# Optimization experiments

Hardware: AMD Instinct MI355X
Metric: run time of the kernel (lower is better)

The kernel has to match this reference:

```python
import jax, jax.numpy as jnp
import numpy as np

B, I, O, G = 4096, 256, 256, 8
GRID_MIN, GRID_MAX, RHO = -2.0, 2.0, 1.0


def setup_inputs() -> dict:
    key = jax.random.key(0)
    ks = jax.random.split(key, 8)
    return {
        "x_re": jax.random.normal(ks[0], (B, I), dtype=jnp.float32),
        "x_im": jax.random.normal(ks[1], (B, I), dtype=jnp.float32),
        "realweights": jax.random.normal(ks[2], (I, O, G, G), dtype=jnp.float32),
        "complexweights": jax.random.normal(ks[3], (I, O, G, G), dtype=jnp.float32),
        "silu_weight_re": jax.random.normal(ks[4], (I, O), dtype=jnp.float32),
        "silu_weight_im": jax.random.normal(ks[5], (I, O), dtype=jnp.float32),
        "silu_bias_re": 0.1 * jax.random.normal(ks[6], (I, O), dtype=jnp.float32),
        "silu_bias_im": 0.1 * jax.random.normal(ks[7], (I, O), dtype=jnp.float32),
    }


def reference(x_re, x_im, realweights, complexweights,
              silu_weight_re, silu_weight_im, silu_bias_re, silu_bias_im):
    # Complex grid: grid[u, v] = lin[u] + i * lin[v]
    lin = jnp.linspace(GRID_MIN, GRID_MAX, G, dtype=x_re.dtype)
    # |x - grid|^2 = (x_re - lin_u)^2 + (x_im - lin_v)^2  -> (B, I, G, G)
    dre = x_re[:, :, None, None] - lin[None, None, :, None]
    dim = x_im[:, :, None, None] - lin[None, None, None, :]
    basis = jnp.exp(-(dre * dre + dim * dim) / RHO)  # real-valued (B, I, G, G)
    # RBF contraction: real and imaginary output channels
    out_re = jnp.einsum('biuv,iouv->bo', basis, realweights)
    out_im = jnp.einsum('biuv,iouv->bo', basis, complexweights)
    # Complex SiLU (complex_weight variant): silu applied component-wise,
    # then complex-multiplied by silu_weight, plus bias, summed over i.
    s_re = jax.nn.silu(x_re)  # (B, I)
    s_im = jax.nn.silu(x_im)
    out_re = out_re + s_re @ silu_weight_re - s_im @ silu_weight_im + jnp.sum(silu_bias_re, axis=0)
    out_im = out_im + s_im @ silu_weight_re + s_re @ silu_weight_im + jnp.sum(silu_bias_im, axis=0)
    # Return complex output as stacked (real, imag): (B, O, 2)
    return jnp.stack([out_re, out_im], axis=-1)
```

## Files before the change

### kernel.cpp

```cpp
#include <hip/hip_runtime.h>
#include <hip/hip_fp16.h>
#include <stdint.h>

typedef float floatx4 __attribute__((ext_vector_type(4)));
typedef short short8 __attribute__((ext_vector_type(8)));

constexpr int I_SZ = 256, O_SZ = 256, NCOL = 512, B_SZ = 4096;
constexpr int KSTEPS = 264;
constexpr float GSTEP = 4.0f / 7.0f;
constexpr float NLOG2E = -1.44269504088896f;

__device__ __forceinline__ uint32_t pk_bf16(float lo, float hi) {
  return __builtin_amdgcn_perm(__float_as_uint(hi), __float_as_uint(lo), 0x07060302u);
}
__device__ __forceinline__ short rne_bf16(float f) {
  uint32_t u = __float_as_uint(f);
  return (short)((u + 0x7FFFu + ((u >> 16) & 1u)) >> 16);
}

__device__ __forceinline__ void gload_lds16(const void* g, void* l) {
  __builtin_amdgcn_global_load_lds((const __attribute__((address_space(1))) void*)g,
                                   (__attribute__((address_space(3))) void*)l,
                                   16, 0, 0);
}

__device__ __forceinline__ float silu_f(float a) {
  return a * __builtin_amdgcn_rcpf(1.f + __builtin_amdgcn_exp2f(a * NLOG2E));
}

__global__ void pack_weights(const float* __restrict__ rw, const float* __restrict__ cw,
                             const float* __restrict__ swre, const float* __restrict__ swim,
                             short* __restrict__ wpack) {
  int idx = blockIdx.x * 256 + threadIdx.x;
  int kb = idx >> 12;
  int rem = idx & 4095;
  int n = rem >> 3, gp = rem & 7;
  int g = gp ^ (n & 7);
  int o = n >> 1, c = n & 1;
  float w[8];
  if (kb < 256) {
    const float* W = (c ? cw : rw) + (((size_t)kb * O_SZ + o) << 6) + (g << 3);
    float4 a = *(const float4*)W;
    float4 b = *(const float4*)(W + 4);
    w[0] = a.x; w[1] = a.y; w[2] = a.z; w[3] = a.w;
    w[4] = b.x; w[5] = b.y; w[6] = b.z; w[7] = b.w;
  } else {
    int kp0 = ((kb - 256) << 6) + (g << 3);
    #pragma unroll
    for (int e = 0; e < 8; ++e) {
      int kp = kp0 + e, i = kp >> 1, ci = kp & 1;
      float a = swre[i * O_SZ + o], b = swim[i * O_SZ + o];
      w[e] = (c == 0) ? (ci == 0 ? a : -b) : (ci == 0 ? b : a);
    }
  }
  uint32_t h[8];
  #pragma unroll
  for (int e = 0; e < 8; ++e) h[e] = (uint32_t)(uint16_t)rne_bf16(w[e]);
  uint4 val = make_uint4(h[0] | (h[1] << 16), h[2] | (h[3] << 16),
                         h[4] | (h[5] << 16), h[6] | (h[7] << 16));
  *(uint4*)(wpack + (size_t)idx * 8) = val;
}

__global__ void transpose_x(const float* __restrict__ xre, const float* __restrict__ xim,
                            __half* __restrict__ xT) {
  __shared__ float tile[64][65];
  int bt = blockIdx.x & 63;
  int it = (blockIdx.x >> 6) & 3;
  int c  = blockIdx.x >> 8;
  const float* src = (c ? xim : xre);
  int b0 = bt << 6, i0 = it << 6;
  int t = threadIdx.x;
  int il = t & 63, bh = t >> 6;
  #pragma unroll
  for (int k = 0; k < 16; ++k) {
    int bl = bh + (k << 2);
    tile[bl][il] = src[(size_t)(b0 + bl) * I_SZ + i0 + il];
  }
  __syncthreads();
  int bl2 = t & 63, ih = t >> 6;
  __half* dst = xT + ((size_t)c * I_SZ + i0) * B_SZ + b0;
  #pragma unroll
  for (int k = 0; k < 16; ++k) {
    int il2 = ih + (k << 2);
    dst[(size_t)il2 * B_SZ + bl2] = __float2half(tile[bl2][il2]);
  }
}

__global__ void bias_sums(const float* __restrict__ bre, const float* __restrict__ bim,
                          float* __restrict__ bsum) {
  int n = blockIdx.x, o = n >> 1, l = threadIdx.x;
  const float* src = ((n & 1) ? bim : bre) + o;
  float s = 0.f;
  #pragma unroll
  for (int a = 0; a < 4; ++a) s += src[(size_t)(a * 64 + l) * O_SZ];
  #pragma unroll
  for (int off = 32; off; off >>= 1) s += __shfl_down(s, off, 64);
  if (l == 0) bsum[n] = s;
}

__global__ __launch_bounds__(256, 4) void cvkan_gemm(
    const float* __restrict__ xre, const float* __restrict__ xim,
    const __half* __restrict__ xT,
    const short* __restrict__ wpack, const float* __restrict__ bsum,
    float* __restrict__ out) {
  __shared__ __align__(16) short Bs[128 * 64];
  __shared__ __align__(16) short As[128 * 64];

  const int tid = threadIdx.x;
  const int bid = blockIdx.x;
  const int kch = bid & 7;
  const int mn = bid >> 3;
  const int mt = mn >> 2, nt = mn & 3;
  const int b0 = mt * 128, n0 = nt * 128;
  const int l = tid & 63, w = tid >> 6;
  const int wr = w >> 1, wc = w & 1;
  const int lm = l & 15, q = l >> 4;
  const int r = tid >> 1, h = tid & 1;

  const __half* xTre = xT;
  const __half* xTim = xT + (size_t)I_SZ * B_SZ;

  floatx4 acc[4][4] = {};

  for (int j = 0; j < 33; ++j) {
    const int s = (j < 32) ? (kch * 32 + j) : (256 + kch);

    float xr = 0.f, xi = 0.f;
    if (j < 32) {
      xr = __half2float(xTre[(size_t)s * B_SZ + b0 + r]);
      xi = __half2float(xTim[(size_t)s * B_SZ + b0 + r]);
    }

    {
      const short* src = wpack + (((size_t)s * NCOL + n0) << 6) + (tid << 3);
      short* ldst = Bs + (w << 9);
      gload_lds16(src,        ldst);
      gload_lds16(src + 2048, ldst + 2048);
      gload_lds16(src + 4096, ldst + 4096);
      gload_lds16(src + 6144, ldst + 6144);
    }

    if (j < 32) {
      float eiv[8];
      #pragma unroll
      for (int v = 0; v < 8; ++v) {
        float d = xi - (-2.0f + v * GSTEP);
        eiv[v] = __builtin_amdgcn_exp2f(d * d * NLOG2E);
      }
      #pragma unroll
      for (int uu = 0; uu < 4; ++uu) {
        int u = h * 4 + uu;
        float d = xr - (-2.0f + u * GSTEP);
        float er = __builtin_amdgcn_exp2f(d * d * NLOG2E);
        uint4 val = make_uint4(pk_bf16(er * eiv[0], er * eiv[1]),
                               pk_bf16(er * eiv[2], er * eiv[3]),
                               pk_bf16(er * eiv[4], er * eiv[5]),
                               pk_bf16(er * eiv[6], er * eiv[7]));
        *(uint4*)(As + (r << 6) + ((u ^ (r & 7)) << 3)) = val;
      }
    } else {
      int sl = kch;
      #pragma unroll
      for (int gg = 0; gg < 4; ++gg) {
        int g = h * 4 + gg;
        const float* pr = xre + (size_t)(b0 + r) * I_SZ + (sl << 5) + (g << 2);
        const float* pi = xim + (size_t)(b0 + r) * I_SZ + (sl << 5) + (g << 2);
        uint4 val = make_uint4(pk_bf16(silu_f(pr[0]), silu_f(pi[0])),
                               pk_bf16(silu_f(pr[1]), silu_f(pi[1])),
                               pk_bf16(silu_f(pr[2]), silu_f(pi[2])),
                               pk_bf16(silu_f(pr[3]), silu_f(pi[3])));
        *(uint4*)(As + (r << 6) + ((g ^ (r & 7)) << 3)) = val;
      }
    }

    __builtin_amdgcn_s_waitcnt(0);
    __syncthreads();

    short8 bf[4][2];
    #pragma unroll
    for (int nn = 0; nn < 4; ++nn) {
      int col = wc * 64 + nn * 16 + lm;
      const short* bp = Bs + (col << 6);
      bf[nn][0] = *(const short8*)(bp + ((q       ^ (col & 7)) << 3));
      bf[nn][1] = *(const short8*)(bp + (((q + 4) ^ (col & 7)) << 3));
    }
    #pragma unroll
    for (int mm = 0; mm < 4; ++mm) {
      int row = wr * 64 + mm * 16 + lm;
      const short* ap = As + (row << 6);
      short8 a0 = *(const short8*)(ap + ((q       ^ (row & 7)) << 3));
      short8 a1 = *(const short8*)(ap + (((q + 4) ^ (row & 7)) << 3));
      #pragma unroll
      for (int nn = 0; nn < 4; ++nn) {
        acc[mm][nn] = __builtin_amdgcn_mfma_f32_16x16x32_bf16(a0, bf[nn][0], acc[mm][nn], 0, 0, 0);
        acc[mm][nn] = __builtin_amdgcn_mfma_f32_16x16x32_bf16(a1, bf[nn][1], acc[mm][nn], 0, 0, 0);
      }
    }
    __syncthreads();
  }

  #pragma unroll
  for (int nn = 0; nn < 4; ++nn) {
    int col = n0 + wc * 64 + nn * 16 + lm;
    float bv = (kch == 7) ? bsum[col] : 0.0f;
    #pragma unroll
    for (int mm = 0; mm < 4; ++mm) {
      int row0 = b0 + wr * 64 + mm * 16 + (q << 2);
      #pragma unroll
      for (int r2 = 0; r2 < 4; ++r2)
        atomicAdd(out + (size_t)(row0 + r2) * NCOL + col, acc[mm][nn][r2] + bv);
    }
  }
}

extern "C" void kernel_launch(void* const* d_in, const int* in_sizes, int n_in,
                              void* d_out, int out_size, void* d_ws, size_t ws_size,
                              hipStream_t stream) {
  const float* xre  = (const float*)d_in[0];
  const float* xim  = (const float*)d_in[1];
  const float* rw   = (const float*)d_in[2];
  const float* cw   = (const float*)d_in[3];
  const float* swre = (const float*)d_in[4];
  const float* swim = (const float*)d_in[5];
  const float* bre  = (const float*)d_in[6];
  const float* bim  = (const float*)d_in[7];
  float* out = (float*)d_out;

  size_t wpack_bytes = (size_t)KSTEPS * NCOL * 64 * 2;
  short* wpack = (short*)d_ws;
  float* bsum  = (float*)((char*)d_ws + wpack_bytes);
  __half* xT   = (__half*)((char*)d_ws + wpack_bytes + 2048);

  hipMemsetAsync(d_out, 0, (size_t)B_SZ * NCOL * sizeof(float), stream);
  pack_weights<<<(KSTEPS * NCOL * 8) / 256, 256, 0, stream>>>(rw, cw, swre, swim, wpack);
  transpose_x<<<512, 256, 0, stream>>>(xre, xim, xT);
  bias_sums<<<NCOL, 64, 0, stream>>>(bre, bim, bsum);
  cvkan_gemm<<<1024, 256, 0, stream>>>(xre, xim, xT, wpack, bsum, out);
}
```

Baseline: 207.5 us.

## Enlarge GEMM tiles to 128x256 and software-pipeline A/B staging

The main kernel now uses 512-thread blocks with a 128x256 output tile and a 4-way K split instead of 8, so the grid drops from 1024 blocks to 256. B tiles are triple-buffered through direct global-to-LDS loads, and A (RBF basis) tiles are double-buffered and built one step ahead. Each step ends with a partial vmcnt wait and a single barrier instead of a full drain and two syncs, and MFMA priority is raised during compute. The aim is to overlap weight loads and basis generation with matrix math and to halve the atomic output traffic. In exchange, more LDS is used per block and only 256 blocks run, which may underfill the GPU.

```diff
diff --git a/kernel.cpp b/kernel.cpp
--- a/kernel.cpp
+++ b/kernel.cpp
@@ -98,49 +98,48 @@
   if (l == 0) bsum[n] = s;
 }
 
-__global__ __launch_bounds__(256, 4) void cvkan_gemm(
+__global__ __launch_bounds__(512, 2) void cvkan_gemm(
     const float* __restrict__ xre, const float* __restrict__ xim,
     const __half* __restrict__ xT,
     const short* __restrict__ wpack, const float* __restrict__ bsum,
     float* __restrict__ out) {
-  __shared__ __align__(16) short Bs[128 * 64];
-  __shared__ __align__(16) short As[128 * 64];
+  __shared__ __align__(16) short As[2 * 128 * 64];
+  __shared__ __align__(16) short Bs[3 * 256 * 64];
 
   const int tid = threadIdx.x;
   const int bid = blockIdx.x;
-  const int kch = bid & 7;
-  const int mn = bid >> 3;
-  const int mt = mn >> 2, nt = mn & 3;
-  const int b0 = mt * 128, n0 = nt * 128;
+  const int kch = bid & 3;
+  const int mn = bid >> 2;
+  const int mt = mn >> 1, nt = mn & 1;
+  const int b0 = mt * 128, n0 = nt * 256;
   const int l = tid & 63, w = tid >> 6;
-  const int wr = w >> 1, wc = w & 1;
+  const int wr = w >> 2, wc = w & 3;
   const int lm = l & 15, q = l >> 4;
-  const int r = tid >> 1, h = tid & 1;
+  const int r = tid >> 2, p = tid & 3;
 
   const __half* xTre = xT;
   const __half* xTim = xT + (size_t)I_SZ * B_SZ;
 
+  short* ac = As;       short* an  = As + 8192;
+  short* bc = Bs;       short* bn1 = Bs + 16384;   short* bn2 = Bs + 32768;
+
   floatx4 acc[4][4] = {};
 
-  for (int j = 0; j < 33; ++j) {
-    const int s = (j < 32) ? (kch * 32 + j) : (256 + kch);
-
-    float xr = 0.f, xi = 0.f;
-    if (j < 32) {
-      xr = __half2float(xTre[(size_t)s * B_SZ + b0 + r]);
-      xi = __half2float(xTim[(size_t)s * B_SZ + b0 + r]);
-    }
-
-    {
-      const short* src = wpack + (((size_t)s * NCOL + n0) << 6) + (tid << 3);
-      short* ldst = Bs + (w << 9);
-      gload_lds16(src,        ldst);
-      gload_lds16(src + 2048, ldst + 2048);
-      gload_lds16(src + 4096, ldst + 4096);
-      gload_lds16(src + 6144, ldst + 6144);
-    }
-
-    if (j < 32) {
+  auto sidx = [&](int j) { return j < 64 ? kch * 64 + j : 256 + kch * 2 + (j - 64); };
+
+  auto stage_B = [&](short* bdst, int s) {
+    const short* src = wpack + (((size_t)s * NCOL + n0) << 6) + (tid << 3);
+    short* ldst = bdst + (w << 9);
+    gload_lds16(src,         ldst);
+    gload_lds16(src +  4096, ldst +  4096);
+    gload_lds16(src +  8192, ldst +  8192);
+    gload_lds16(src + 12288, ldst + 12288);
+  };
+
+  auto build_A = [&](short* adst, int s) {
+    if (s < 256) {
+      float xr = __half2float(xTre[(size_t)s * B_SZ + b0 + r]);
+      float xi = __half2float(xTim[(size_t)s * B_SZ + b0 + r]);
       float eiv[8];
       #pragma unroll
       for (int v = 0; v < 8; ++v) {
@@ -148,46 +147,55 @@
         eiv[v] = __builtin_amdgcn_exp2f(d * d * NLOG2E);
       }
       #pragma unroll
-      for (int uu = 0; uu < 4; ++uu) {
-        int u = h * 4 + uu;
+      for (int uu = 0; uu < 2; ++uu) {
+        int u = p * 2 + uu;
         float d = xr - (-2.0f + u * GSTEP);
         float er = __builtin_amdgcn_exp2f(d * d * NLOG2E);
         uint4 val = make_uint4(pk_bf16(er * eiv[0], er * eiv[1]),
                                pk_bf16(er * eiv[2], er * eiv[3]),
                                pk_bf16(er * eiv[4], er * eiv[5]),
                                pk_bf16(er * eiv[6], er * eiv[7]));
-        *(uint4*)(As + (r << 6) + ((u ^ (r & 7)) << 3)) = val;
+        *(uint4*)(adst + (r << 6) + ((u ^ (r & 7)) << 3)) = val;
       }
     } else {
-      int sl = kch;
-      #pragma unroll
-      for (int gg = 0; gg < 4; ++gg) {
-        int g = h * 4 + gg;
+      int sl = s - 256;
+      #pragma unroll
+      for (int gg = 0; gg < 2; ++gg) {
+        int g = p * 2 + gg;
         const float* pr = xre + (size_t)(b0 + r) * I_SZ + (sl << 5) + (g << 2);
         const float* pi = xim + (size_t)(b0 + r) * I_SZ + (sl << 5) + (g << 2);
         uint4 val = make_uint4(pk_bf16(silu_f(pr[0]), silu_f(pi[0])),
                                pk_bf16(silu_f(pr[1]), silu_f(pi[1])),
                                pk_bf16(silu_f(pr[2]), silu_f(pi[2])),
                                pk_bf16(silu_f(pr[3]), silu_f(pi[3])));
-        *(uint4*)(As + (r << 6) + ((g ^ (r & 7)) << 3)) = val;
-      }
-    }
-
-    __builtin_amdgcn_s_waitcnt(0);
-    __syncthreads();
+        *(uint4*)(adst + (r << 6) + ((g ^ (r & 7)) << 3)) = val;
+      }
+    }
+  };
+
+  stage_B(bc, sidx(0));
+  stage_B(bn1, sidx(1));
+  build_A(ac, sidx(0));
+  asm volatile("s_waitcnt vmcnt(4) lgkmcnt(0)" ::: "memory");
+  __builtin_amdgcn_s_barrier();
+
+  for (int j = 0; j < 66; ++j) {
+    if (j < 64) stage_B(bn2, sidx(j + 2));
+    if (j < 65) build_A(an, sidx(j + 1));
 
     short8 bf[4][2];
     #pragma unroll
     for (int nn = 0; nn < 4; ++nn) {
       int col = wc * 64 + nn * 16 + lm;
-      const short* bp = Bs + (col << 6);
+      const short* bp = bc + (col << 6);
       bf[nn][0] = *(const short8*)(bp + ((q       ^ (col & 7)) << 3));
       bf[nn][1] = *(const short8*)(bp + (((q + 4) ^ (col & 7)) << 3));
     }
+    __builtin_amdgcn_s_setprio(1);
     #pragma unroll
     for (int mm = 0; mm < 4; ++mm) {
       int row = wr * 64 + mm * 16 + lm;
-      const short* ap = As + (row << 6);
+      const short* ap = ac + (row << 6);
       short8 a0 = *(const short8*)(ap + ((q       ^ (row & 7)) << 3));
       short8 a1 = *(const short8*)(ap + (((q + 4) ^ (row & 7)) << 3));
       #pragma unroll
@@ -196,13 +204,21 @@
         acc[mm][nn] = __builtin_amdgcn_mfma_f32_16x16x32_bf16(a1, bf[nn][1], acc[mm][nn], 0, 0, 0);
       }
     }
-    __syncthreads();
+    __builtin_amdgcn_s_setprio(0);
+
+    if (j < 65) {
+      if (j < 64) asm volatile("s_waitcnt vmcnt(4) lgkmcnt(0)" ::: "memory");
+      else        asm volatile("s_waitcnt vmcnt(0) lgkmcnt(0)" ::: "memory");
+      __builtin_amdgcn_s_barrier();
+    }
+    short* t = bc; bc = bn1; bn1 = bn2; bn2 = t;
+    t = ac; ac = an; an = t;
   }
 
   #pragma unroll
   for (int nn = 0; nn < 4; ++nn) {
     int col = n0 + wc * 64 + nn * 16 + lm;
-    float bv = (kch == 7) ? bsum[col] : 0.0f;
+    float bv = (kch == 3) ? bsum[col] : 0.0f;
     #pragma unroll
     for (int mm = 0; mm < 4; ++mm) {
       int row0 = b0 + wr * 64 + mm * 16 + (q << 2);
@@ -235,5 +251,5 @@
   pack_weights<<<(KSTEPS * NCOL * 8) / 256, 256, 0, stream>>>(rw, cw, swre, swim, wpack);
   transpose_x<<<512, 256, 0, stream>>>(xre, xim, xT);
   bias_sums<<<NCOL, 64, 0, stream>>>(bre, bim, bsum);
-  cvkan_gemm<<<1024, 256, 0, stream>>>(xre, xim, xT, wpack, bsum, out);
-}
+  cvkan_gemm<<<256, 512, 0, stream>>>(xre, xim, xT, wpack, bsum, out);
+}
```

Result: slower. 223.0 us (+7.5%).

## Double-buffer B tiles and compute next A tile in registers during MFMA

Applied to the files above, without the earlier changes.

Double-buffers the weight tile in LDS so the async global-to-LDS load for the next K-step is issued before the current step's MFMAs. The next step's RBF basis is computed into registers while the MFMAs run, and x values are prefetched one step ahead. The global load is then waited on with a partial vmcnt instead of a full drain, and s_setprio raises wave priority around the MFMA block. The larger LDS footprint lowers the launch bound from 4 to 3 blocks per CU, so occupancy may drop and the hand-written waitcnt counts must stay exactly right.

```diff
diff --git a/kernel.cpp b/kernel.cpp
--- a/kernel.cpp
+++ b/kernel.cpp
@@ -98,13 +98,13 @@
   if (l == 0) bsum[n] = s;
 }
 
-__global__ __launch_bounds__(256, 4) void cvkan_gemm(
+__global__ __launch_bounds__(256, 3) void cvkan_gemm(
     const float* __restrict__ xre, const float* __restrict__ xim,
     const __half* __restrict__ xT,
     const short* __restrict__ wpack, const float* __restrict__ bsum,
     float* __restrict__ out) {
-  __shared__ __align__(16) short Bs[128 * 64];
   __shared__ __align__(16) short As[128 * 64];
+  __shared__ __align__(16) short Bs[2 * 128 * 64];
 
   const int tid = threadIdx.x;
   const int bid = blockIdx.x;
@@ -121,26 +121,21 @@
   const __half* xTim = xT + (size_t)I_SZ * B_SZ;
 
   floatx4 acc[4][4] = {};
-
-  for (int j = 0; j < 33; ++j) {
-    const int s = (j < 32) ? (kch * 32 + j) : (256 + kch);
-
-    float xr = 0.f, xi = 0.f;
-    if (j < 32) {
-      xr = __half2float(xTre[(size_t)s * B_SZ + b0 + r]);
-      xi = __half2float(xTim[(size_t)s * B_SZ + b0 + r]);
-    }
-
-    {
-      const short* src = wpack + (((size_t)s * NCOL + n0) << 6) + (tid << 3);
-      short* ldst = Bs + (w << 9);
-      gload_lds16(src,        ldst);
-      gload_lds16(src + 2048, ldst + 2048);
-      gload_lds16(src + 4096, ldst + 4096);
-      gload_lds16(src + 6144, ldst + 6144);
-    }
-
-    if (j < 32) {
+  uint4 rA[4];
+
+  auto sidx = [&](int j) { return (j < 32) ? (kch * 32 + j) : (256 + kch); };
+
+  auto stage_B = [&](short* bdst, int s) {
+    const short* src = wpack + (((size_t)s * NCOL + n0) << 6) + (tid << 3);
+    short* ldst = bdst + (w << 9);
+    gload_lds16(src,        ldst);
+    gload_lds16(src + 2048, ldst + 2048);
+    gload_lds16(src + 4096, ldst + 4096);
+    gload_lds16(src + 6144, ldst + 6144);
+  };
+
+  auto build_A = [&](int s, float xr, float xi) {
+    if (s < 256) {
       float eiv[8];
       #pragma unroll
       for (int v = 0; v < 8; ++v) {
@@ -152,38 +147,73 @@
         int u = h * 4 + uu;
         float d = xr - (-2.0f + u * GSTEP);
         float er = __builtin_amdgcn_exp2f(d * d * NLOG2E);
-        uint4 val = make_uint4(pk_bf16(er * eiv[0], er * eiv[1]),
-                               pk_bf16(er * eiv[2], er * eiv[3]),
-                               pk_bf16(er * eiv[4], er * eiv[5]),
-                               pk_bf16(er * eiv[6], er * eiv[7]));
-        *(uint4*)(As + (r << 6) + ((u ^ (r & 7)) << 3)) = val;
+        rA[uu] = make_uint4(pk_bf16(er * eiv[0], er * eiv[1]),
+                            pk_bf16(er * eiv[2], er * eiv[3]),
+                            pk_bf16(er * eiv[4], er * eiv[5]),
+                            pk_bf16(er * eiv[6], er * eiv[7]));
       }
     } else {
-      int sl = kch;
+      int sl = s - 256;
       #pragma unroll
       for (int gg = 0; gg < 4; ++gg) {
         int g = h * 4 + gg;
         const float* pr = xre + (size_t)(b0 + r) * I_SZ + (sl << 5) + (g << 2);
         const float* pi = xim + (size_t)(b0 + r) * I_SZ + (sl << 5) + (g << 2);
-        uint4 val = make_uint4(pk_bf16(silu_f(pr[0]), silu_f(pi[0])),
-                               pk_bf16(silu_f(pr[1]), silu_f(pi[1])),
-                               pk_bf16(silu_f(pr[2]), silu_f(pi[2])),
-                               pk_bf16(silu_f(pr[3]), silu_f(pi[3])));
-        *(uint4*)(As + (r << 6) + ((g ^ (r & 7)) << 3)) = val;
-      }
-    }
-
-    __builtin_amdgcn_s_waitcnt(0);
-    __syncthreads();
+        rA[gg] = make_uint4(pk_bf16(silu_f(pr[0]), silu_f(pi[0])),
+                            pk_bf16(silu_f(pr[1]), silu_f(pi[1])),
+                            pk_bf16(silu_f(pr[2]), silu_f(pi[2])),
+                            pk_bf16(silu_f(pr[3]), silu_f(pi[3])));
+      }
+    }
+  };
+
+  auto write_A = [&]() {
+    #pragma unroll
+    for (int uu = 0; uu < 4; ++uu) {
+      int u = h * 4 + uu;
+      *(uint4*)(As + (r << 6) + ((u ^ (r & 7)) << 3)) = rA[uu];
+    }
+  };
+
+  stage_B(Bs, sidx(0));
+  {
+    int s0 = sidx(0);
+    float xr = __half2float(xTre[(size_t)s0 * B_SZ + b0 + r]);
+    float xi = __half2float(xTim[(size_t)s0 * B_SZ + b0 + r]);
+    build_A(s0, xr, xi);
+  }
+
+  short* bcur = Bs;
+  short* bnxt = Bs + 8192;
+
+  for (int j = 0; j <= 32; ++j) {
+    const int sn = sidx(j + 1);
+
+    float xrn = 0.f, xin = 0.f;
+    if (j < 32 && sn < 256) {
+      xrn = __half2float(xTre[(size_t)sn * B_SZ + b0 + r]);
+      xin = __half2float(xTim[(size_t)sn * B_SZ + b0 + r]);
+    }
+    __builtin_amdgcn_sched_barrier(0);
+
+    if (j < 32) stage_B(bnxt, sn);
+    write_A();
+
+    if (j < 32) asm volatile("s_waitcnt vmcnt(4) lgkmcnt(0)" ::: "memory");
+    else        asm volatile("s_waitcnt vmcnt(0) lgkmcnt(0)" ::: "memory");
+    __builtin_amdgcn_s_barrier();
+
+    if (j < 32) build_A(sn, xrn, xin);
 
     short8 bf[4][2];
     #pragma unroll
     for (int nn = 0; nn < 4; ++nn) {
       int col = wc * 64 + nn * 16 + lm;
-      const short* bp = Bs + (col << 6);
+      const short* bp = bcur + (col << 6);
       bf[nn][0] = *(const short8*)(bp + ((q       ^ (col & 7)) << 3));
       bf[nn][1] = *(const short8*)(bp + (((q + 4) ^ (col & 7)) << 3));
     }
+    __builtin_amdgcn_s_setprio(1);
     #pragma unroll
     for (int mm = 0; mm < 4; ++mm) {
       int row = wr * 64 + mm * 16 + lm;
@@ -196,7 +226,10 @@
         acc[mm][nn] = __builtin_amdgcn_mfma_f32_16x16x32_bf16(a1, bf[nn][1], acc[mm][nn], 0, 0, 0);
       }
     }
-    __syncthreads();
+    __builtin_amdgcn_s_setprio(0);
+
+    if (j < 32) __builtin_amdgcn_s_barrier();
+    short* t = bcur; bcur = bnxt; bnxt = t;
   }
 
   #pragma unroll
```

Result: slower. 228.1 us (+9.9%).

## Double-buffer weight tiles, compute RBF A-fragments in registers, widen N tile

Applied to the files above, without the earlier changes.

The GEMM now uses a 128x256 output tile per block with two LDS buffers for the weight tile, prefetching the next K-step's weights and x values while the current step runs its MFMAs. The RBF basis is computed directly into A-operand registers per lane, so the A shared-memory tile and one barrier per step go away. MFMAs are wrapped in s_setprio. The aim is to overlap loads with compute and cut LDS traffic and syncs. In exchange there are more accumulators and registers, occupancy drops to 2 blocks, the grid is halved, and lanes sharing a row recompute exp values redundantly.

```diff
diff --git a/kernel.cpp b/kernel.cpp
--- a/kernel.cpp
+++ b/kernel.cpp
@@ -98,110 +98,138 @@
   if (l == 0) bsum[n] = s;
 }
 
-__global__ __launch_bounds__(256, 4) void cvkan_gemm(
+__global__ __launch_bounds__(256, 2) void cvkan_gemm(
     const float* __restrict__ xre, const float* __restrict__ xim,
     const __half* __restrict__ xT,
     const short* __restrict__ wpack, const float* __restrict__ bsum,
     float* __restrict__ out) {
-  __shared__ __align__(16) short Bs[128 * 64];
-  __shared__ __align__(16) short As[128 * 64];
+  __shared__ __align__(16) short Bs[2][256 * 64];
 
   const int tid = threadIdx.x;
   const int bid = blockIdx.x;
   const int kch = bid & 7;
   const int mn = bid >> 3;
-  const int mt = mn >> 2, nt = mn & 3;
-  const int b0 = mt * 128, n0 = nt * 128;
+  const int mt = mn >> 1, nt = mn & 1;
+  const int b0 = mt * 128, n0 = nt * 256;
   const int l = tid & 63, w = tid >> 6;
   const int wr = w >> 1, wc = w & 1;
   const int lm = l & 15, q = l >> 4;
-  const int r = tid >> 1, h = tid & 1;
+  const float gq  = -2.0f + q * GSTEP;
+  const float gq4 = gq + 4.0f * GSTEP;
 
   const __half* xTre = xT;
   const __half* xTim = xT + (size_t)I_SZ * B_SZ;
 
-  floatx4 acc[4][4] = {};
-
-  for (int j = 0; j < 33; ++j) {
-    const int s = (j < 32) ? (kch * 32 + j) : (256 + kch);
-
-    float xr = 0.f, xi = 0.f;
-    if (j < 32) {
-      xr = __half2float(xTre[(size_t)s * B_SZ + b0 + r]);
-      xi = __half2float(xTim[(size_t)s * B_SZ + b0 + r]);
-    }
-
-    {
-      const short* src = wpack + (((size_t)s * NCOL + n0) << 6) + (tid << 3);
-      short* ldst = Bs + (w << 9);
-      gload_lds16(src,        ldst);
-      gload_lds16(src + 2048, ldst + 2048);
-      gload_lds16(src + 4096, ldst + 4096);
-      gload_lds16(src + 6144, ldst + 6144);
-    }
-
-    if (j < 32) {
-      float eiv[8];
-      #pragma unroll
-      for (int v = 0; v < 8; ++v) {
-        float d = xi - (-2.0f + v * GSTEP);
-        eiv[v] = __builtin_amdgcn_exp2f(d * d * NLOG2E);
+  floatx4 acc[4][8] = {};
+
+  auto stage_B = [&](short* bdst, int s) {
+    const short* src = wpack + (((size_t)s * NCOL + n0) << 6) + (tid << 3);
+    short* ldst = bdst + (w << 9);
+    #pragma unroll
+    for (int rnd = 0; rnd < 8; ++rnd)
+      gload_lds16(src + rnd * 2048, ldst + rnd * 2048);
+  };
+
+  float xrc[4], xic[4];
+  auto load_x = [&](int s, float* xr, float* xi) {
+    #pragma unroll
+    for (int mm = 0; mm < 4; ++mm) {
+      int row = b0 + wr * 64 + mm * 16 + lm;
+      xr[mm] = __half2float(xTre[(size_t)s * B_SZ + row]);
+      xi[mm] = __half2float(xTim[(size_t)s * B_SZ + row]);
+    }
+  };
+
+  {
+    int s0 = kch * 32;
+    load_x(s0, xrc, xic);
+    stage_B(&Bs[0][0], s0);
+    asm volatile("s_waitcnt vmcnt(0) lgkmcnt(0)" ::: "memory");
+  }
+  __syncthreads();
+
+  for (int t = 0; t < 33; ++t) {
+    const bool last = (t == 32);
+    float xrn[4], xin[4];
+    if (t < 31) load_x(kch * 32 + t + 1, xrn, xin);
+    if (t < 32) stage_B(&Bs[(t + 1) & 1][0], (t + 1 < 32) ? (kch * 32 + t + 1) : (256 + kch));
+    __builtin_amdgcn_sched_barrier(0);
+
+    const short* bb = &Bs[t & 1][0];
+
+    short8 bf[8];
+    #pragma unroll
+    for (int nn = 0; nn < 8; ++nn) {
+      int colL = wc * 128 + nn * 16 + lm;
+      bf[nn] = *(const short8*)(bb + (colL << 6) + ((q ^ (colL & 7)) << 3));
+    }
+    short8 afh[4];
+    #pragma unroll
+    for (int mm = 0; mm < 4; ++mm) {
+      short8 alo;
+      if (!last) {
+        float eiv[8];
+        #pragma unroll
+        for (int v = 0; v < 8; ++v) {
+          float d = xic[mm] - (-2.0f + v * GSTEP);
+          eiv[v] = __builtin_amdgcn_exp2f(d * d * NLOG2E);
+        }
+        float d0 = xrc[mm] - gq;
+        float er = __builtin_amdgcn_exp2f(d0 * d0 * NLOG2E);
+        float d1 = xrc[mm] - gq4;
+        float e4 = __builtin_amdgcn_exp2f(d1 * d1 * NLOG2E);
+        uint4 va = make_uint4(pk_bf16(er * eiv[0], er * eiv[1]), pk_bf16(er * eiv[2], er * eiv[3]),
+                              pk_bf16(er * eiv[4], er * eiv[5]), pk_bf16(er * eiv[6], er * eiv[7]));
+        uint4 vh = make_uint4(pk_bf16(e4 * eiv[0], e4 * eiv[1]), pk_bf16(e4 * eiv[2], e4 * eiv[3]),
+                              pk_bf16(e4 * eiv[4], e4 * eiv[5]), pk_bf16(e4 * eiv[6], e4 * eiv[7]));
+        alo = *(short8*)&va; afh[mm] = *(short8*)&vh;
+      } else {
+        int row = b0 + wr * 64 + mm * 16 + lm;
+        const float* pr = xre + (size_t)row * I_SZ + (kch << 5);
+        const float* pi = xim + (size_t)row * I_SZ + (kch << 5);
+        uint4 va = make_uint4(pk_bf16(silu_f(pr[q * 4 + 0]), silu_f(pi[q * 4 + 0])),
+                              pk_bf16(silu_f(pr[q * 4 + 1]), silu_f(pi[q * 4 + 1])),
+                              pk_bf16(silu_f(pr[q * 4 + 2]), silu_f(pi[q * 4 + 2])),
+                              pk_bf16(silu_f(pr[q * 4 + 3]), silu_f(pi[q * 4 + 3])));
+        uint4 vh = make_uint4(pk_bf16(silu_f(pr[q * 4 + 16]), silu_f(pi[q * 4 + 16])),
+                              pk_bf16(silu_f(pr[q * 4 + 17]), silu_f(pi[q * 4 + 17])),
+                              pk_bf16(silu_f(pr[q * 4 + 18]), silu_f(pi[q * 4 + 18])),
+                              pk_bf16(silu_f(pr[q * 4 + 19]), silu_f(pi[q * 4 + 19])));
+        alo = *(short8*)&va; afh[mm] = *(short8*)&vh;
       }
-      #pragma unroll
-      for (int uu = 0; uu < 4; ++uu) {
-        int u = h * 4 + uu;
-        float d = xr - (-2.0f + u * GSTEP);
-        float er = __builtin_amdgcn_exp2f(d * d * NLOG2E);
-        uint4 val = make_uint4(pk_bf16(er * eiv[0], er * eiv[1]),
-                               pk_bf16(er * eiv[2], er * eiv[3]),
-                               pk_bf16(er * eiv[4], er * eiv[5]),
-                               pk_bf16(er * eiv[6], er * eiv[7]));
-        *(uint4*)(As + (r << 6) + ((u ^ (r & 7)) << 3)) = val;
-      }
-    } else {
-      int sl = kch;
-      #pragma unroll
-      for (int gg = 0; gg < 4; ++gg) {
-        int g = h * 4 + gg;
-        const float* pr = xre + (size_t)(b0 + r) * I_SZ + (sl << 5) + (g << 2);
-        const float* pi = xim + (size_t)(b0 + r) * I_SZ + (sl << 5) + (g << 2);
-        uint4 val = make_uint4(pk_bf16(silu_f(pr[0]), silu_f(pi[0])),
-                               pk_bf16(silu_f(pr[1]), silu_f(pi[1])),
-                               pk_bf16(silu_f(pr[2]), silu_f(pi[2])),
-                               pk_bf16(silu_f(pr[3]), silu_f(pi[3])));
-        *(uint4*)(As + (r << 6) + ((g ^ (r & 7)) << 3)) = val;
-      }
-    }
-
-    __builtin_amdgcn_s_waitcnt(0);
-    __syncthreads();
-
-    short8 bf[4][2];
-    #pragma unroll
-    for (int nn = 0; nn < 4; ++nn) {
-      int col = wc * 64 + nn * 16 + lm;
-      const short* bp = Bs + (col << 6);
-      bf[nn][0] = *(const short8*)(bp + ((q       ^ (col & 7)) << 3));
-      bf[nn][1] = *(const short8*)(bp + (((q + 4) ^ (col & 7)) << 3));
-    }
-    #pragma unroll
-    for (int mm = 0; mm < 4; ++mm) {
-      int row = wr * 64 + mm * 16 + lm;
-      const short* ap = As + (row << 6);
-      short8 a0 = *(const short8*)(ap + ((q       ^ (row & 7)) << 3));
-      short8 a1 = *(const short8*)(ap + (((q + 4) ^ (row & 7)) << 3));
-      #pragma unroll
-      for (int nn = 0; nn < 4; ++nn) {
-        acc[mm][nn] = __builtin_amdgcn_mfma_f32_16x16x32_bf16(a0, bf[nn][0], acc[mm][nn], 0, 0, 0);
-        acc[mm][nn] = __builtin_amdgcn_mfma_f32_16x16x32_bf16(a1, bf[nn][1], acc[mm][nn], 0, 0, 0);
-      }
-    }
-    __syncthreads();
-  }
-
-  #pragma unroll
-  for (int nn = 0; nn < 4; ++nn) {
-    int col = n0 + wc * 64 + nn * 16 + lm;
+      __builtin_amdgcn_s_setprio(1);
+      #pragma unroll
+      for (int nn = 0; nn < 8; ++nn)
+        acc[mm][nn] = __builtin_amdgcn_mfma_f32_16x16x32_bf16(alo, bf[nn], acc[mm][nn], 0, 0, 0);
+      __builtin_amdgcn_s_setprio(0);
+    }
+
+    #pragma unroll
+    for (int nn = 0; nn < 8; ++nn) {
+      int colL = wc * 128 + nn * 16 + lm;
+      bf[nn] = *(const short8*)(bb + (colL << 6) + (((q + 4) ^ (colL & 7)) << 3));
+    }
+    __builtin_amdgcn_s_setprio(1);
+    #pragma unroll
+    for (int mm = 0; mm < 4; ++mm)
+      #pragma unroll
+      for (int nn = 0; nn < 8; ++nn)
+        acc[mm][nn] = __builtin_amdgcn_mfma_f32_16x16x32_bf16(afh[mm], bf[nn], acc[mm][nn], 0, 0, 0);
+    __builtin_amdgcn_s_setprio(0);
+
+    if (t < 31) {
+      #pragma unroll
+      for (int mm = 0; mm < 4; ++mm) { xrc[mm] = xrn[mm]; xic[mm] = xin[mm]; }
+    }
+    if (t < 32) {
+      asm volatile("s_waitcnt vmcnt(0) lgkmcnt(0)" ::: "memory");
+      __syncthreads();
+    }
+  }
+
+  #pragma unroll
+  for (int nn = 0; nn < 8; ++nn) {
+    int col = n0 + wc * 128 + nn * 16 + lm;
     float bv = (kch == 7) ? bsum[col] : 0.0f;
     #pragma unroll
     for (int mm = 0; mm < 4; ++mm) {
@@ -235,5 +263,5 @@
   pack_weights<<<(KSTEPS * NCOL * 8) / 256, 256, 0, stream>>>(rw, cw, swre, swim, wpack);
   transpose_x<<<512, 256, 0, stream>>>(xre, xim, xT);
   bias_sums<<<NCOL, 64, 0, stream>>>(bre, bim, bsum);
-  cvkan_gemm<<<1024, 256, 0, stream>>>(xre, xim, xT, wpack, bsum, out);
-}
+  cvkan_gemm<<<512, 256, 0, stream>>>(xre, xim, xT, wpack, bsum, out);
+}
```

Result: slower. 221.0 us (+6.5%).
